# Performance work log

Measured on AMD Instinct MI355X. Metric: run time of the kernel, lower is better.

Reference implementation:

```python
import jax, jax.numpy as jnp
import numpy as np

N, E, F_NODE, F_EDGE, H, L, G = 4096, 12288, 64, 16, 128, 4, 256
BN_EPS = 1e-5


def setup_inputs() -> dict:
    key = jax.random.key(0)
    ks = jax.random.split(key, 20)
    s = lambda k, shape, fan: jax.random.normal(k, shape, jnp.float32) * (1.0 / np.sqrt(fan))
    inp = {
        'x': jax.random.normal(ks[0], (N, F_NODE), jnp.float32),
        'edge_index': jax.random.randint(ks[1], (2, E), 0, N, dtype=jnp.int64),
        'edge_attr': jax.random.normal(ks[2], (E, F_EDGE), jnp.float32),
        'batch': jnp.sort(jax.random.randint(ks[3], (N,), 0, G, dtype=jnp.int64)),
        # node encoder
        'node_w': s(ks[4], (F_NODE, H), F_NODE),
        'node_b': jnp.zeros((H,), jnp.float32),
        # per-layer edge MLP: edge_feat -> 128 -> H*H
        'e1_w': s(ks[5], (L, F_EDGE, 128), F_EDGE),
        'e1_b': jnp.zeros((L, 128), jnp.float32),
        'e2_w': s(ks[6], (L, 128, H * H), 128) * 0.1,
        'e2_b': jnp.zeros((L, H * H), jnp.float32),
        # NNConv root weight + bias
        'root_w': s(ks[7], (L, H, H), H),
        'conv_b': jnp.zeros((L, H), jnp.float32),
        # batchnorm affine
        'bn_g': jnp.ones((L, H), jnp.float32),
        'bn_b': jnp.zeros((L, H), jnp.float32),
        # head
        'head_w1': s(ks[8], (H, H), H),
        'head_b1': jnp.zeros((H,), jnp.float32),
        'head_w2': s(ks[9], (H, 1), H),
        'head_b2': jnp.zeros((1,), jnp.float32),
    }
    return inp


def reference(x, edge_index, edge_attr, batch, node_w, node_b, e1_w, e1_b,
              e2_w, e2_b, root_w, conv_b, bn_g, bn_b, head_w1, head_b1,
              head_w2, head_b2):
    src, dst = edge_index[0], edge_index[1]
    h = x @ node_w + node_b  # [N,H]
    # in-degree for mean aggregation
    deg = jax.ops.segment_sum(jnp.ones((E,), h.dtype), dst, num_segments=N)
    inv_deg = jnp.where(deg > 0, 1.0 / jnp.maximum(deg, 1.0), 0.0)[:, None]
    for l in range(L):
        # edge MLP -> per-edge [H,H] weight
        e = jax.nn.relu(edge_attr @ e1_w[l] + e1_b[l])            # [E,128]
        W_e = (e @ e2_w[l] + e2_b[l]).reshape(E, H, H)            # [E,H,H]
        msg = jnp.einsum('eh,eho->eo', h[src], W_e)               # [E,H]
        agg = jax.ops.segment_sum(msg, dst, num_segments=N) * inv_deg
        out = agg + h @ root_w[l] + conv_b[l]
        # batchnorm (training-mode batch stats, biased var as in torch)
        mu = out.mean(0)
        var = out.var(0)
        out = (out - mu) * jax.lax.rsqrt(var + BN_EPS) * bn_g[l] + bn_b[l]
        h = h + jax.nn.relu(out)  # dropout disabled (eval)
    # global mean pool over graphs
    cnt = jax.ops.segment_sum(jnp.ones((N,), h.dtype), batch, num_segments=G)
    pooled = jax.ops.segment_sum(h, batch, num_segments=G) / jnp.maximum(cnt, 1.0)[:, None]
    y = jax.nn.relu(pooled @ head_w1 + head_b1) @ head_w2 + head_b2
    return y.squeeze(-1)  # [G]
```

## Files before the change

### kernel.cpp

```cpp
#include <hip/hip_runtime.h>

#define N_NODES 4096
#define E_TOT   12288
#define F_NODE  64
#define F_EDGE  16
#define HDIM    128
#define NLAYER  4
#define NGRAPH  256

typedef _Float16 half8 __attribute__((ext_vector_type(8)));
typedef float    f32x4 __attribute__((ext_vector_type(4)));

__global__ void k_prep_w2(const float* __restrict__ e2w, const float* __restrict__ e2b,
                          _Float16* __restrict__ W2F)
{
    int t = blockIdx.x * 256 + threadIdx.x;
    const int PER_L = 129 * 16384;
    if (t >= NLAYER * PER_L) return;
    int l   = t / PER_L;
    int r   = t - l * PER_L;
    int k   = r >> 14;
    int rem = r & 16383;
    int chunk = rem >> 9;
    int lane  = (rem >> 3) & 63;
    int j     = rem & 7;
    int hc = chunk >> 3, ot = chunk & 7;
    int h  = hc * 32 + (lane >> 4) * 8 + j;
    int o  = ot * 16 + (lane & 15);
    float v;
    if (k < 128) v = e2w[((size_t)(l * 128 + k)) * 16384 + h * 128 + o];
    else         v = e2b[(size_t)l * 16384 + h * 128 + o];
    W2F[t] = (_Float16)v;
}

__global__ __launch_bounds__(128)
void k_node_enc(const float* __restrict__ x, const float* __restrict__ nw,
                const float* __restrict__ nb, float* __restrict__ h,
                _Float16* __restrict__ hf)
{
    __shared__ float xl[F_NODE];
    int n = blockIdx.x, o = threadIdx.x;
    if (o < F_NODE) xl[o] = x[(size_t)n * F_NODE + o];
    __syncthreads();
    float acc = nb[o];
#pragma unroll 8
    for (int f = 0; f < F_NODE; ++f) acc += xl[f] * nw[f * HDIM + o];
    h [(size_t)n * HDIM + o] = acc;
    hf[(size_t)n * HDIM + o] = (_Float16)acc;
}

__global__ void k_deg(const int* __restrict__ dst, int* __restrict__ deg)
{
    int e = blockIdx.x * 256 + threadIdx.x;
    if (e < E_TOT) atomicAdd(&deg[dst[e]], 1);
}

__global__ void k_invd(const int* __restrict__ deg, float* __restrict__ invd)
{
    int n = blockIdx.x * 256 + threadIdx.x;
    if (n < N_NODES) invd[n] = deg[n] > 0 ? 1.0f / (float)deg[n] : 0.0f;
}

#define EF_STRIDE 136
__global__ __launch_bounds__(256)
void k_edge_mlp(const float* __restrict__ ea, const float* __restrict__ w1,
                const float* __restrict__ b1, _Float16* __restrict__ efg)
{
    __shared__ float al[16][17];
    __shared__ float wl[16][HDIM];
    __shared__ float bl[HDIM];
    int t = threadIdx.x, e0 = blockIdx.x * 16;
    if (t < HDIM) bl[t] = b1[t];
    for (int i = t; i < F_EDGE * HDIM; i += 256) wl[i >> 7][i & 127] = w1[i];
    { int i = t; al[i >> 4][i & 15] = ea[(size_t)e0 * F_EDGE + i]; }
    __syncthreads();
    int e = t >> 4, og = t & 15;
    float acc[8];
#pragma unroll
    for (int j = 0; j < 8; ++j) acc[j] = bl[og * 8 + j];
#pragma unroll
    for (int f = 0; f < F_EDGE; ++f) {
        float a = al[e][f];
#pragma unroll
        for (int j = 0; j < 8; ++j) acc[j] += a * wl[f][og * 8 + j];
    }
    half8 o;
#pragma unroll
    for (int j = 0; j < 8; ++j) o[j] = (_Float16)fmaxf(acc[j], 0.f);
    *(half8*)&efg[(size_t)(e0 + e) * EF_STRIDE + og * 8] = o;
    if (og == 0) efg[(size_t)(e0 + e) * EF_STRIDE + 128] = (_Float16)1.0f;
}

#define BM 64
__global__ __launch_bounds__(256, 3)
void k_msg(const _Float16* __restrict__ W2L,
           const _Float16* __restrict__ efg,
           const _Float16* __restrict__ hf,
           const int* __restrict__ srcIdx,
           const int* __restrict__ dstIdx,
           float* __restrict__ agg4)
{
    __shared__ _Float16 efs[BM][40];

    const int tid  = threadIdx.x;
    const int lane = tid & 63;
    const int w    = tid >> 6;
    const int lhi  = lane >> 4;
    const int llo  = lane & 15;

    const int bx    = blockIdx.x;
    const int ks    = (bx & 7) >> 1;
    const int tile  = (bx >> 3) * 2 + (bx & 1);
    const int e0    = tile * BM;
    const int kbase = (129 * ks) >> 2;
    const int kcnt  = ((129 * (ks + 1)) >> 2) - kbase;
    float* agg = agg4 + (size_t)ks * N_NODES * HDIM;

    for (int i = tid; i < BM * 5; i += 256) {
        int r = i / 5, c = i - r * 5;
        *(half8*)&efs[r][c * 8] =
            *(const half8*)(efg + (size_t)(e0 + r) * EF_STRIDE + kbase + c * 8);
    }

    half8 hs[4][4];
#pragma unroll
    for (int rf = 0; rf < 4; ++rf) {
        int s = srcIdx[e0 + rf * 16 + llo];
        const _Float16* hp = hf + (size_t)s * HDIM + lhi * 8;
#pragma unroll
        for (int hc = 0; hc < 4; ++hc)
            hs[rf][hc] = *(const half8*)(hp + hc * 32);
    }

    __syncthreads();

    const _Float16* bp = W2L + (size_t)kbase * 16384 + (w * 2) * 512 + lane * 8;

#define LDH(dst, kk, h2) do {                                          \
        const _Float16* p_ = bp + (size_t)(kk) * 16384 + (h2) * 8192;  \
        dst[0] = *(const half8*)(p_);                                  \
        dst[1] = *(const half8*)(p_ + 512);                            \
        dst[2] = *(const half8*)(p_ + 4096);                           \
        dst[3] = *(const half8*)(p_ + 4608);                           \
    } while (0)

    half8 B0[4], B1[4];
    LDH(B0, 0, 0);
    LDH(B1, 0, 1);

    f32x4 acc[4][2];
#pragma unroll
    for (int rf = 0; rf < 4; ++rf)
#pragma unroll
        for (int cf = 0; cf < 2; ++cf)
#pragma unroll
            for (int d = 0; d < 4; ++d) acc[rf][cf][d] = 0.f;

    for (int kk = 0; kk < kcnt; ++kk) {
        _Float16 efv[4];
#pragma unroll
        for (int rf = 0; rf < 4; ++rf) efv[rf] = efs[rf * 16 + llo][kk];

#pragma unroll
        for (int rf = 0; rf < 4; ++rf) {
            half8 av0 = hs[rf][0] * efv[rf];
            half8 av1 = hs[rf][1] * efv[rf];
            acc[rf][0] = __builtin_amdgcn_mfma_f32_16x16x32_f16(av0, B0[0], acc[rf][0], 0, 0, 0);
            acc[rf][1] = __builtin_amdgcn_mfma_f32_16x16x32_f16(av0, B0[1], acc[rf][1], 0, 0, 0);
            acc[rf][0] = __builtin_amdgcn_mfma_f32_16x16x32_f16(av1, B0[2], acc[rf][0], 0, 0, 0);
            acc[rf][1] = __builtin_amdgcn_mfma_f32_16x16x32_f16(av1, B0[3], acc[rf][1], 0, 0, 0);
        }
        if (kk + 1 < kcnt) LDH(B0, kk + 1, 0);

#pragma unroll
        for (int rf = 0; rf < 4; ++rf) {
            half8 av2 = hs[rf][2] * efv[rf];
            half8 av3 = hs[rf][3] * efv[rf];
            acc[rf][0] = __builtin_amdgcn_mfma_f32_16x16x32_f16(av2, B1[0], acc[rf][0], 0, 0, 0);
            acc[rf][1] = __builtin_amdgcn_mfma_f32_16x16x32_f16(av2, B1[1], acc[rf][1], 0, 0, 0);
            acc[rf][0] = __builtin_amdgcn_mfma_f32_16x16x32_f16(av3, B1[2], acc[rf][0], 0, 0, 0);
            acc[rf][1] = __builtin_amdgcn_mfma_f32_16x16x32_f16(av3, B1[3], acc[rf][1], 0, 0, 0);
        }
        if (kk + 1 < kcnt) LDH(B1, kk + 1, 1);
    }
#undef LDH

#pragma unroll
    for (int rf = 0; rf < 4; ++rf) {
#pragma unroll
        for (int r = 0; r < 4; ++r) {
            int row = rf * 16 + lhi * 4 + r;
            int d   = dstIdx[e0 + row];
#pragma unroll
            for (int cf = 0; cf < 2; ++cf) {
                int o = w * 32 + cf * 16 + llo;
                atomicAdd(&agg[(size_t)d * HDIM + o], acc[rf][cf][r]);
            }
        }
    }
}

__global__ __launch_bounds__(128)
void k_out(const float* __restrict__ agg4, const float* __restrict__ invd,
           const float* __restrict__ h, const float* __restrict__ rw,
           const float* __restrict__ cb, float* __restrict__ outb,
           float* __restrict__ bns1, float* __restrict__ bns2)
{
    __shared__ float hl[16][HDIM];
    int n0 = blockIdx.x * 16, o = threadIdx.x;
    for (int r = 0; r < 16; ++r) hl[r][o] = h[(size_t)(n0 + r) * HDIM + o];
    __syncthreads();
    float acc[16];
    float cbv = cb[o];
#pragma unroll
    for (int r = 0; r < 16; ++r) {
        float s = 0.f;
#pragma unroll
        for (int p = 0; p < 4; ++p)
            s += agg4[(size_t)p * N_NODES * HDIM + (size_t)(n0 + r) * HDIM + o];
        acc[r] = s * invd[n0 + r] + cbv;
    }
    for (int hh = 0; hh < HDIM; ++hh) {
        float wv = rw[hh * HDIM + o];
#pragma unroll
        for (int r = 0; r < 16; ++r) acc[r] += hl[r][hh] * wv;
    }
    float s1 = 0.f, s2 = 0.f;
#pragma unroll
    for (int r = 0; r < 16; ++r) {
        outb[(size_t)(n0 + r) * HDIM + o] = acc[r];
        s1 += acc[r];
        s2 += acc[r] * acc[r];
    }
    atomicAdd(&bns1[o], s1);
    atomicAdd(&bns2[o], s2);
}

__global__ void k_bn_apply(const float* __restrict__ outb, const float* __restrict__ bns1,
                           const float* __restrict__ bns2, const float* __restrict__ g,
                           const float* __restrict__ b, float* __restrict__ h,
                           _Float16* __restrict__ hf)
{
    int i = blockIdx.x * 256 + threadIdx.x;
    int o = i & (HDIM - 1);
    const float inv_n = 1.0f / (float)N_NODES;
    float m   = bns1[o] * inv_n;
    float var = bns2[o] * inv_n - m * m;
    float rs  = rsqrtf(var + 1e-5f);
    float v  = (outb[i] - m) * rs * g[o] + b[o];
    float hn = h[i] + fmaxf(v, 0.f);
    h[i]  = hn;
    hf[i] = (_Float16)hn;
}

__global__ __launch_bounds__(128)
void k_pool(const float* __restrict__ h, const int* __restrict__ batch,
            float* __restrict__ pooled, int* __restrict__ cnt)
{
    int n = blockIdx.x, c = threadIdx.x;
    int g = batch[n];
    atomicAdd(&pooled[(size_t)g * HDIM + c], h[(size_t)n * HDIM + c]);
    if (c == 0) atomicAdd(&cnt[g], 1);
}

__global__ __launch_bounds__(128)
void k_head(const float* __restrict__ pooled, const int* __restrict__ cnt,
            const float* __restrict__ w1, const float* __restrict__ b1,
            const float* __restrict__ w2, const float* __restrict__ b2,
            float* __restrict__ y)
{
    __shared__ float pl[HDIM];
    __shared__ float red[HDIM];
    int g = blockIdx.x, o = threadIdx.x;
    float ic = 1.0f / (float)max(cnt[g], 1);
    pl[o] = pooled[(size_t)g * HDIM + o] * ic;
    __syncthreads();
    float t = b1[o];
#pragma unroll 8
    for (int hh = 0; hh < HDIM; ++hh) t += pl[hh] * w1[hh * HDIM + o];
    t = fmaxf(t, 0.f);
    red[o] = t * w2[o];
    __syncthreads();
    for (int s = 64; s > 0; s >>= 1) {
        if (o < s) red[o] += red[o + s];
        __syncthreads();
    }
    if (o == 0) y[g] = red[0] + b2[0];
}

extern "C" void kernel_launch(void* const* d_in, const int* in_sizes, int n_in,
                              void* d_out, int out_size, void* d_ws, size_t ws_size,
                              hipStream_t stream)
{
    const float* x      = (const float*)d_in[0];
    const int*   ei     = (const int*)  d_in[1];
    const float* ea     = (const float*)d_in[2];
    const int*   batch  = (const int*)  d_in[3];
    const float* node_w = (const float*)d_in[4];
    const float* node_b = (const float*)d_in[5];
    const float* e1w    = (const float*)d_in[6];
    const float* e1b    = (const float*)d_in[7];
    const float* e2w    = (const float*)d_in[8];
    const float* e2b    = (const float*)d_in[9];
    const float* rw     = (const float*)d_in[10];
    const float* cb     = (const float*)d_in[11];
    const float* bng    = (const float*)d_in[12];
    const float* bnb    = (const float*)d_in[13];
    const float* hw1    = (const float*)d_in[14];
    const float* hb1    = (const float*)d_in[15];
    const float* hw2    = (const float*)d_in[16];
    const float* hb2    = (const float*)d_in[17];
    float* y = (float*)d_out;

    char* ws = (char*)d_ws;
    _Float16* W2F  = (_Float16*)ws; ws += 16908288;
    float*    h    = (float*)ws;    ws += 2097152;
    _Float16* hf   = (_Float16*)ws; ws += 1048576;
    _Float16* efg  = (_Float16*)ws; ws += 3342336;
    float*    agg4 = (float*)ws;    ws += 8388608;
    float*    bns1 = (float*)ws;    ws += 512;
    float*    bns2 = (float*)ws;    ws += 512;
    float*    outb = (float*)ws;    ws += 2097152;
    int*      deg  = (int*)ws;      ws += 16384;
    float*    invd = (float*)ws;    ws += 16384;
    float*    pooled = (float*)ws;  ws += 131072;
    int*      cnt  = (int*)ws;      ws += 1024;

    const int* src = ei;
    const int* dst = ei + E_TOT;

    k_prep_w2<<<33024, 256, 0, stream>>>(e2w, e2b, W2F);
    k_node_enc<<<N_NODES, 128, 0, stream>>>(x, node_w, node_b, h, hf);
    hipMemsetAsync(deg, 0, N_NODES * sizeof(int), stream);
    k_deg<<<(E_TOT + 255) / 256, 256, 0, stream>>>(dst, deg);
    k_invd<<<(N_NODES + 255) / 256, 256, 0, stream>>>(deg, invd);

    for (int l = 0; l < NLAYER; ++l) {
        k_edge_mlp<<<E_TOT / 16, 256, 0, stream>>>(ea, e1w + l * F_EDGE * HDIM,
                                                   e1b + l * HDIM, efg);
        hipMemsetAsync(agg4, 0, (size_t)4 * N_NODES * HDIM * sizeof(float) + 1024, stream);
        k_msg<<<(E_TOT / BM) * 4, 256, 0, stream>>>(W2F + (size_t)l * 129 * 16384,
                                                    efg, hf, src, dst, agg4);
        k_out<<<N_NODES / 16, 128, 0, stream>>>(agg4, invd, h,
                                                rw + l * HDIM * HDIM,
                                                cb + l * HDIM, outb, bns1, bns2);
        k_bn_apply<<<(N_NODES * HDIM) / 256, 256, 0, stream>>>(
            outb, bns1, bns2, bng + l * HDIM, bnb + l * HDIM, h, hf);
    }

    hipMemsetAsync(pooled, 0, (size_t)NGRAPH * HDIM * sizeof(float), stream);
    hipMemsetAsync(cnt, 0, NGRAPH * sizeof(int), stream);
    k_pool<<<N_NODES, 128, 0, stream>>>(h, batch, pooled, cnt);
    k_head<<<NGRAPH, 128, 0, stream>>>(pooled, cnt, hw1, hb1, hw2, hb2, y);
}
```

Baseline: 432.2 us.

## Merge split-K aggregation buffers, fuse memsets and pooling into existing kernels

The four per-split aggregation buffers become one shared buffer that all K-splits atomically add into. The per-layer memset disappears: the BN-apply kernel re-zeroes agg, k_msg zeroes the BN stat accumulators, and the final pooling is folded into the last BN-apply. The message loop is restructured to prefetch B fragments in four quarter-chunks and to preload the next edge-feature scalar. This removes launches, memset traffic and a 4x larger reduction read, at the cost of more atomic contention on a single buffer.

```diff
diff --git a/kernel.cpp b/kernel.cpp
--- a/kernel.cpp
+++ b/kernel.cpp
@@ -98,7 +98,9 @@
            const _Float16* __restrict__ hf,
            const int* __restrict__ srcIdx,
            const int* __restrict__ dstIdx,
-           float* __restrict__ agg4)
+           float* __restrict__ agg,
+           float* __restrict__ bns1,
+           float* __restrict__ bns2)
 {
     __shared__ _Float16 efs[BM][40];
 
@@ -114,7 +116,11 @@
     const int e0    = tile * BM;
     const int kbase = (129 * ks) >> 2;
     const int kcnt  = ((129 * (ks + 1)) >> 2) - kbase;
-    float* agg = agg4 + (size_t)ks * N_NODES * HDIM;
+
+    if (bx == 0) {
+        if (tid < HDIM)            bns1[tid] = 0.f;
+        else if (tid < 2 * HDIM)   bns2[tid - HDIM] = 0.f;
+    }
 
     for (int i = tid; i < BM * 5; i += 256) {
         int r = i / 5, c = i - r * 5;
@@ -136,17 +142,16 @@
 
     const _Float16* bp = W2L + (size_t)kbase * 16384 + (w * 2) * 512 + lane * 8;
 
-#define LDH(dst, kk, h2) do {                                          \
-        const _Float16* p_ = bp + (size_t)(kk) * 16384 + (h2) * 8192;  \
-        dst[0] = *(const half8*)(p_);                                  \
-        dst[1] = *(const half8*)(p_ + 512);                            \
-        dst[2] = *(const half8*)(p_ + 4096);                           \
-        dst[3] = *(const half8*)(p_ + 4608);                           \
+#define LDQ(d0, d1, kk, hc) do {                                            \
+        const _Float16* p_ = bp + (size_t)(kk) * 16384 + (hc) * 4096;       \
+        d0 = *(const half8*)(p_); d1 = *(const half8*)(p_ + 512);           \
     } while (0)
 
-    half8 B0[4], B1[4];
-    LDH(B0, 0, 0);
-    LDH(B1, 0, 1);
+    half8 b00, b01, b10, b11, b20, b21, b30, b31;
+    LDQ(b00, b01, 0, 0);
+    LDQ(b10, b11, 0, 1);
+    LDQ(b20, b21, 0, 2);
+    LDQ(b30, b31, 0, 3);
 
     f32x4 acc[4][2];
 #pragma unroll
@@ -156,34 +161,53 @@
 #pragma unroll
             for (int d = 0; d < 4; ++d) acc[rf][cf][d] = 0.f;
 
+    _Float16 efc[4];
+#pragma unroll
+    for (int rf = 0; rf < 4; ++rf) efc[rf] = efs[rf * 16 + llo][0];
+
     for (int kk = 0; kk < kcnt; ++kk) {
-        _Float16 efv[4];
-#pragma unroll
-        for (int rf = 0; rf < 4; ++rf) efv[rf] = efs[rf * 16 + llo][kk];
+        const bool nx = (kk + 1 < kcnt);
+        _Float16 efn[4];
+        const int kn = nx ? kk + 1 : kk;
+#pragma unroll
+        for (int rf = 0; rf < 4; ++rf) efn[rf] = efs[rf * 16 + llo][kn];
 
 #pragma unroll
         for (int rf = 0; rf < 4; ++rf) {
-            half8 av0 = hs[rf][0] * efv[rf];
-            half8 av1 = hs[rf][1] * efv[rf];
-            acc[rf][0] = __builtin_amdgcn_mfma_f32_16x16x32_f16(av0, B0[0], acc[rf][0], 0, 0, 0);
-            acc[rf][1] = __builtin_amdgcn_mfma_f32_16x16x32_f16(av0, B0[1], acc[rf][1], 0, 0, 0);
-            acc[rf][0] = __builtin_amdgcn_mfma_f32_16x16x32_f16(av1, B0[2], acc[rf][0], 0, 0, 0);
-            acc[rf][1] = __builtin_amdgcn_mfma_f32_16x16x32_f16(av1, B0[3], acc[rf][1], 0, 0, 0);
-        }
-        if (kk + 1 < kcnt) LDH(B0, kk + 1, 0);
+            half8 av = hs[rf][0] * efc[rf];
+            acc[rf][0] = __builtin_amdgcn_mfma_f32_16x16x32_f16(av, b00, acc[rf][0], 0, 0, 0);
+            acc[rf][1] = __builtin_amdgcn_mfma_f32_16x16x32_f16(av, b01, acc[rf][1], 0, 0, 0);
+        }
+        if (nx) LDQ(b00, b01, kk + 1, 0);
 
 #pragma unroll
         for (int rf = 0; rf < 4; ++rf) {
-            half8 av2 = hs[rf][2] * efv[rf];
-            half8 av3 = hs[rf][3] * efv[rf];
-            acc[rf][0] = __builtin_amdgcn_mfma_f32_16x16x32_f16(av2, B1[0], acc[rf][0], 0, 0, 0);
-            acc[rf][1] = __builtin_amdgcn_mfma_f32_16x16x32_f16(av2, B1[1], acc[rf][1], 0, 0, 0);
-            acc[rf][0] = __builtin_amdgcn_mfma_f32_16x16x32_f16(av3, B1[2], acc[rf][0], 0, 0, 0);
-            acc[rf][1] = __builtin_amdgcn_mfma_f32_16x16x32_f16(av3, B1[3], acc[rf][1], 0, 0, 0);
-        }
-        if (kk + 1 < kcnt) LDH(B1, kk + 1, 1);
-    }
-#undef LDH
+            half8 av = hs[rf][1] * efc[rf];
+            acc[rf][0] = __builtin_amdgcn_mfma_f32_16x16x32_f16(av, b10, acc[rf][0], 0, 0, 0);
+            acc[rf][1] = __builtin_amdgcn_mfma_f32_16x16x32_f16(av, b11, acc[rf][1], 0, 0, 0);
+        }
+        if (nx) LDQ(b10, b11, kk + 1, 1);
+
+#pragma unroll
+        for (int rf = 0; rf < 4; ++rf) {
+            half8 av = hs[rf][2] * efc[rf];
+            acc[rf][0] = __builtin_amdgcn_mfma_f32_16x16x32_f16(av, b20, acc[rf][0], 0, 0, 0);
+            acc[rf][1] = __builtin_amdgcn_mfma_f32_16x16x32_f16(av, b21, acc[rf][1], 0, 0, 0);
+        }
+        if (nx) LDQ(b20, b21, kk + 1, 2);
+
+#pragma unroll
+        for (int rf = 0; rf < 4; ++rf) {
+            half8 av = hs[rf][3] * efc[rf];
+            acc[rf][0] = __builtin_amdgcn_mfma_f32_16x16x32_f16(av, b30, acc[rf][0], 0, 0, 0);
+            acc[rf][1] = __builtin_amdgcn_mfma_f32_16x16x32_f16(av, b31, acc[rf][1], 0, 0, 0);
+        }
+        if (nx) LDQ(b30, b31, kk + 1, 3);
+
+#pragma unroll
+        for (int rf = 0; rf < 4; ++rf) efc[rf] = efn[rf];
+    }
+#undef LDQ
 
 #pragma unroll
     for (int rf = 0; rf < 4; ++rf) {
@@ -201,7 +225,7 @@
 }
 
 __global__ __launch_bounds__(128)
-void k_out(const float* __restrict__ agg4, const float* __restrict__ invd,
+void k_out(const float* __restrict__ agg, const float* __restrict__ invd,
            const float* __restrict__ h, const float* __restrict__ rw,
            const float* __restrict__ cb, float* __restrict__ outb,
            float* __restrict__ bns1, float* __restrict__ bns2)
@@ -213,13 +237,8 @@
     float acc[16];
     float cbv = cb[o];
 #pragma unroll
-    for (int r = 0; r < 16; ++r) {
-        float s = 0.f;
-#pragma unroll
-        for (int p = 0; p < 4; ++p)
-            s += agg4[(size_t)p * N_NODES * HDIM + (size_t)(n0 + r) * HDIM + o];
-        acc[r] = s * invd[n0 + r] + cbv;
-    }
+    for (int r = 0; r < 16; ++r)
+        acc[r] = agg[(size_t)(n0 + r) * HDIM + o] * invd[n0 + r] + cbv;
     for (int hh = 0; hh < HDIM; ++hh) {
         float wv = rw[hh * HDIM + o];
 #pragma unroll
@@ -239,7 +258,9 @@
 __global__ void k_bn_apply(const float* __restrict__ outb, const float* __restrict__ bns1,
                            const float* __restrict__ bns2, const float* __restrict__ g,
                            const float* __restrict__ b, float* __restrict__ h,
-                           _Float16* __restrict__ hf)
+                           _Float16* __restrict__ hf, float* __restrict__ agg,
+                           const int* __restrict__ batch, float* __restrict__ pooled,
+                           int* __restrict__ cnt, int last)
 {
     int i = blockIdx.x * 256 + threadIdx.x;
     int o = i & (HDIM - 1);
@@ -251,16 +272,14 @@
     float hn = h[i] + fmaxf(v, 0.f);
     h[i]  = hn;
     hf[i] = (_Float16)hn;
-}
-
-__global__ __launch_bounds__(128)
-void k_pool(const float* __restrict__ h, const int* __restrict__ batch,
-            float* __restrict__ pooled, int* __restrict__ cnt)
-{
-    int n = blockIdx.x, c = threadIdx.x;
-    int g = batch[n];
-    atomicAdd(&pooled[(size_t)g * HDIM + c], h[(size_t)n * HDIM + c]);
-    if (c == 0) atomicAdd(&cnt[g], 1);
+    if (!last) {
+        agg[i] = 0.f;
+    } else {
+        int n  = i >> 7;
+        int gg = batch[n];
+        atomicAdd(&pooled[(size_t)gg * HDIM + o], hn);
+        if (o == 0) atomicAdd(&cnt[gg], 1);
+    }
 }
 
 __global__ __launch_bounds__(128)
@@ -317,7 +336,7 @@
     float*    h    = (float*)ws;    ws += 2097152;
     _Float16* hf   = (_Float16*)ws; ws += 1048576;
     _Float16* efg  = (_Float16*)ws; ws += 3342336;
-    float*    agg4 = (float*)ws;    ws += 8388608;
+    float*    agg  = (float*)ws;    ws += 2097152;
     float*    bns1 = (float*)ws;    ws += 512;
     float*    bns2 = (float*)ws;    ws += 512;
     float*    outb = (float*)ws;    ws += 2097152;
@@ -334,22 +353,21 @@
     hipMemsetAsync(deg, 0, N_NODES * sizeof(int), stream);
     k_deg<<<(E_TOT + 255) / 256, 256, 0, stream>>>(dst, deg);
     k_invd<<<(N_NODES + 255) / 256, 256, 0, stream>>>(deg, invd);
+    hipMemsetAsync(agg, 0, (size_t)N_NODES * HDIM * sizeof(float), stream);
+    hipMemsetAsync(pooled, 0, (size_t)NGRAPH * HDIM * sizeof(float) + NGRAPH * sizeof(int), stream);
 
     for (int l = 0; l < NLAYER; ++l) {
         k_edge_mlp<<<E_TOT / 16, 256, 0, stream>>>(ea, e1w + l * F_EDGE * HDIM,
                                                    e1b + l * HDIM, efg);
-        hipMemsetAsync(agg4, 0, (size_t)4 * N_NODES * HDIM * sizeof(float) + 1024, stream);
         k_msg<<<(E_TOT / BM) * 4, 256, 0, stream>>>(W2F + (size_t)l * 129 * 16384,
-                                                    efg, hf, src, dst, agg4);
-        k_out<<<N_NODES / 16, 128, 0, stream>>>(agg4, invd, h,
+                                                    efg, hf, src, dst, agg, bns1, bns2);
+        k_out<<<N_NODES / 16, 128, 0, stream>>>(agg, invd, h,
                                                 rw + l * HDIM * HDIM,
                                                 cb + l * HDIM, outb, bns1, bns2);
         k_bn_apply<<<(N_NODES * HDIM) / 256, 256, 0, stream>>>(
-            outb, bns1, bns2, bng + l * HDIM, bnb + l * HDIM, h, hf);
-    }
-
-    hipMemsetAsync(pooled, 0, (size_t)NGRAPH * HDIM * sizeof(float), stream);
-    hipMemsetAsync(cnt, 0, NGRAPH * sizeof(int), stream);
-    k_pool<<<N_NODES, 128, 0, stream>>>(h, batch, pooled, cnt);
+            outb, bns1, bns2, bng + l * HDIM, bnb + l * HDIM, h, hf,
+            agg, batch, pooled, cnt, (l == NLAYER - 1) ? 1 : 0);
+    }
+
     k_head<<<NGRAPH, 128, 0, stream>>>(pooled, cnt, hw1, hb1, hw2, hb2, y);
 }
```

Result: faster. 416.5 us (-3.6%).
